# Optimization experiments

Hardware: AMD Instinct MI355X
Metric: run time of the kernel (lower is better)

The kernel has to match this reference:

```python
import jax, jax.numpy as jnp
import numpy as np


def setup_inputs() -> dict:
    key = jax.random.key(0)
    k1, k2, k3 = jax.random.split(key, 3)
    B, S, D_IN, D_OUT = 2, 2048, 4096, 4096
    x = jax.random.normal(k1, (B, S, D_IN), dtype=jnp.float32)
    # int8 quantized weight (stored as int32 container, values in int8 range)
    weight = jax.random.randint(k2, (D_OUT, D_IN), 0, 127, dtype=jnp.int32)
    weight_scaler = jax.random.uniform(k3, (D_OUT,), dtype=jnp.float32)
    return {"x": x, "weight": weight, "weight_scaler": weight_scaler}


def reference(x, weight, weight_scaler):
    # Dequantize per-output-channel: w_fp = int8_weight * scaler[:, None]
    w = weight.astype(jnp.float32) * weight_scaler[:, None]  # [O, I]
    # F.linear: x @ w.T
    return jnp.einsum("bsi,oi->bso", x, w)
```

## Files before the change

### kernel.cpp

```cpp
#include <hip/hip_runtime.h>

typedef int i32x4 __attribute__((ext_vector_type(4)));

#define AS1 __attribute__((address_space(1)))
#define AS3 __attribute__((address_space(3)))

__global__ __launch_bounds__(256) void quant_kernel(
    const float4* __restrict__ x, const int4* __restrict__ w,
    signed char* __restrict__ xq, signed char* __restrict__ wq,
    float* __restrict__ sx, int M, int Kq) {
  const int tid = threadIdx.x;
  if ((int)blockIdx.x < M) {
    const int r = blockIdx.x;
    float4 v[4];
    #pragma unroll
    for (int j = 0; j < 4; ++j) v[j] = x[(size_t)r * 1024 + tid * 4 + j];
    float m = 0.f;
    #pragma unroll
    for (int j = 0; j < 4; ++j)
      m = fmaxf(m, fmaxf(fmaxf(fabsf(v[j].x), fabsf(v[j].y)),
                         fmaxf(fabsf(v[j].z), fabsf(v[j].w))));
    #pragma unroll
    for (int off = 1; off < 64; off <<= 1) m = fmaxf(m, __shfl_xor(m, off));
    __shared__ float wmax[4];
    if ((tid & 63) == 0) wmax[tid >> 6] = m;
    __syncthreads();
    m = fmaxf(fmaxf(wmax[0], wmax[1]), fmaxf(wmax[2], wmax[3]));
    const float inv = (m > 0.f) ? 127.0f / m : 0.f;
    if (tid == 0) sx[r] = m * (1.0f / 127.0f);
    signed char q[16];
    #pragma unroll
    for (int j = 0; j < 4; ++j) {
      q[j * 4 + 0] = (signed char)__float2int_rn(v[j].x * inv);
      q[j * 4 + 1] = (signed char)__float2int_rn(v[j].y * inv);
      q[j * 4 + 2] = (signed char)__float2int_rn(v[j].z * inv);
      q[j * 4 + 3] = (signed char)__float2int_rn(v[j].w * inv);
    }
    ((int4*)xq)[(size_t)r * 256 + tid] = *(const int4*)q;
  } else {
    const int b = blockIdx.x - M;
    int4 v[4];
    #pragma unroll
    for (int j = 0; j < 4; ++j) v[j] = w[(size_t)b * 1024 + tid * 4 + j];
    signed char q[16];
    #pragma unroll
    for (int j = 0; j < 4; ++j) {
      q[j * 4 + 0] = (signed char)v[j].x; q[j * 4 + 1] = (signed char)v[j].y;
      q[j * 4 + 2] = (signed char)v[j].z; q[j * 4 + 3] = (signed char)v[j].w;
    }
    ((int4*)wq)[(size_t)b * 256 + tid] = *(const int4*)q;
  }
}

__global__ __launch_bounds__(512, 2) void gemm_i8_kernel(
    const signed char* __restrict__ A,
    const signed char* __restrict__ B,
    const float* __restrict__ sx,
    const float* __restrict__ scaler,
    float* __restrict__ C,
    int M, int N, int K)
{
  __shared__ signed char sA[4][256 * 64];
  __shared__ signed char sB[4][256 * 64];

  const int tid  = threadIdx.x;
  const int wave = tid >> 6;
  const int lane = tid & 63;
  const int bm = blockIdx.y << 8;
  const int bn = blockIdx.x << 8;

  const int wm = (wave >> 2) << 7;
  const int wn = (wave & 3) << 6;
  const int l15  = lane & 15;
  const int quad = lane >> 4;

  const int srow = tid >> 2;
  const int kg = (tid & 3) ^ ((srow >> 1) & 3);
  const signed char* ga = A + (size_t)(bm + srow) * K + kg * 16;
  const signed char* gb = B + (size_t)(bn + srow) * K + kg * 16;
  const size_t rstep = (size_t)128 * K;
  const int ldst = tid * 16;

  const int pk   = (quad ^ ((l15 >> 1) & 3)) << 4;
  const int aoff = (wm + l15) * 64 + pk;
  const int boff = (wn + l15) * 64 + pk;

  i32x4 acc[8][4] = {};

#define STAGE_A(tt) do { const int sb_ = (tt) & 3;                           \
    __builtin_amdgcn_global_load_lds((AS1 void*)(ga + (size_t)(tt) * 64),    \
                                     (AS3 void*)(&sA[sb_][ldst]), 16, 0, 0); \
    __builtin_amdgcn_global_load_lds((AS1 void*)(ga + (size_t)(tt) * 64 + rstep), \
                                     (AS3 void*)(&sA[sb_][8192 + ldst]), 16, 0, 0); } while (0)
#define STAGE_B(tt) do { const int sb_ = (tt) & 3;                           \
    __builtin_amdgcn_global_load_lds((AS1 void*)(gb + (size_t)(tt) * 64),    \
                                     (AS3 void*)(&sB[sb_][ldst]), 16, 0, 0); \
    __builtin_amdgcn_global_load_lds((AS1 void*)(gb + (size_t)(tt) * 64 + rstep), \
                                     (AS3 void*)(&sB[sb_][8192 + ldst]), 16, 0, 0); } while (0)

  const int nt = K >> 6;

  STAGE_A(0); STAGE_B(0); STAGE_A(1); STAGE_B(1);
  asm volatile("s_waitcnt vmcnt(4)" ::: "memory");
  __builtin_amdgcn_s_barrier();
  __builtin_amdgcn_sched_barrier(0);

  for (int t = 0; t < nt; ++t) {
    const signed char* la = sA[t & 3];
    const signed char* lb = sB[t & 3];
    const bool st = (t < nt - 2);
    i32x4 av[4], bv[4];

    if (st) STAGE_A(t + 2);
    #pragma unroll
    for (int ni = 0; ni < 4; ++ni) bv[ni] = *(const i32x4*)&lb[boff + ni * 1024];
    #pragma unroll
    for (int mi = 0; mi < 4; ++mi) av[mi] = *(const i32x4*)&la[aoff + mi * 1024];
    __builtin_amdgcn_s_barrier();
    __builtin_amdgcn_s_setprio(1);
    #pragma unroll
    for (int mi = 0; mi < 4; ++mi)
      #pragma unroll
      for (int ni = 0; ni < 4; ++ni)
        acc[mi][ni] = __builtin_amdgcn_mfma_i32_16x16x64_i8(av[mi], bv[ni], acc[mi][ni], 0, 0, 0);
    __builtin_amdgcn_s_setprio(0);
    __builtin_amdgcn_s_barrier();

    if (st) STAGE_B(t + 2);
    #pragma unroll
    for (int mi = 0; mi < 4; ++mi) av[mi] = *(const i32x4*)&la[aoff + (mi + 4) * 1024];
    __builtin_amdgcn_s_barrier();
    __builtin_amdgcn_s_setprio(1);
    #pragma unroll
    for (int mi = 0; mi < 4; ++mi)
      #pragma unroll
      for (int ni = 0; ni < 4; ++ni)
        acc[mi + 4][ni] = __builtin_amdgcn_mfma_i32_16x16x64_i8(av[mi], bv[ni], acc[mi + 4][ni], 0, 0, 0);
    __builtin_amdgcn_s_setprio(0);

    if (st)                 asm volatile("s_waitcnt vmcnt(4)" ::: "memory");
    else if (t == nt - 2)   asm volatile("s_waitcnt vmcnt(0)" ::: "memory");
    __builtin_amdgcn_s_barrier();
    __builtin_amdgcn_sched_barrier(0);
  }
#undef STAGE_A
#undef STAGE_B

  #pragma unroll
  for (int mi = 0; mi < 8; ++mi) {
    const int gm0 = bm + wm + mi * 16 + quad * 4;
    float sr[4];
    #pragma unroll
    for (int r = 0; r < 4; ++r) sr[r] = sx[gm0 + r];
    #pragma unroll
    for (int ni = 0; ni < 4; ++ni) {
      const int gn = bn + wn + ni * 16 + l15;
      const float sc = scaler[gn];
      #pragma unroll
      for (int r = 0; r < 4; ++r)
        C[(size_t)(gm0 + r) * N + gn] = (float)acc[mi][ni][r] * sr[r] * sc;
    }
  }
}

extern "C" void kernel_launch(void* const* d_in, const int* in_sizes, int n_in,
                              void* d_out, int out_size, void* d_ws, size_t ws_size,
                              hipStream_t stream) {
  const float* x  = (const float*)d_in[0];
  const int*   w  = (const int*)d_in[1];
  const float* sc = (const float*)d_in[2];
  float* out = (float*)d_out;

  const int N = in_sizes[2];
  const int K = in_sizes[1] / N;
  const int M = in_sizes[0] / K;

  signed char* Aq = (signed char*)d_ws;
  signed char* Bq = Aq + (size_t)M * K;
  float* sx = (float*)(Bq + (size_t)N * K);

  const int wBlocks = (N * K) / (256 * 16);
  quant_kernel<<<M + wBlocks, 256, 0, stream>>>(
      (const float4*)x, (const int4*)w, Aq, Bq, sx, M, K / 16);

  dim3 grid(N / 256, M / 256);
  gemm_i8_kernel<<<grid, 512, 0, stream>>>(Aq, Bq, sx, sc, out, M, N, K);
}
```

Before: 252.1 us.

## Deepen LDS prefetch to three stages and use one barrier per K-step

The int8 GEMM main loop now prefetches three K-tiles ahead into the four LDS buffers instead of two. It issues the A and B tile loads together, then loads all eight A fragments and runs all 32 MFMAs in one block. The four per-iteration barriers and the setprio toggles are replaced by a single waitcnt plus barrier. The aim is to hide more global-load latency and cut synchronisation overhead. In exchange it holds more VGPRs for the fragments and loses the split load/compute interleave across waves.

After: 251.2 us. About the same (-0.3%).

```diff
diff --git a/kernel.cpp b/kernel.cpp
--- a/kernel.cpp
+++ b/kernel.cpp
@@ -87,64 +87,46 @@
 
   i32x4 acc[8][4] = {};
 
-#define STAGE_A(tt) do { const int sb_ = (tt) & 3;                           \
-    __builtin_amdgcn_global_load_lds((AS1 void*)(ga + (size_t)(tt) * 64),    \
-                                     (AS3 void*)(&sA[sb_][ldst]), 16, 0, 0); \
-    __builtin_amdgcn_global_load_lds((AS1 void*)(ga + (size_t)(tt) * 64 + rstep), \
-                                     (AS3 void*)(&sA[sb_][8192 + ldst]), 16, 0, 0); } while (0)
-#define STAGE_B(tt) do { const int sb_ = (tt) & 3;                           \
-    __builtin_amdgcn_global_load_lds((AS1 void*)(gb + (size_t)(tt) * 64),    \
-                                     (AS3 void*)(&sB[sb_][ldst]), 16, 0, 0); \
-    __builtin_amdgcn_global_load_lds((AS1 void*)(gb + (size_t)(tt) * 64 + rstep), \
-                                     (AS3 void*)(&sB[sb_][8192 + ldst]), 16, 0, 0); } while (0)
+#define STAGE(tt) do { const int sb_ = (tt) & 3; const size_t ko_ = (size_t)(tt) * 64; \
+    __builtin_amdgcn_global_load_lds((AS1 void*)(ga + ko_),         (AS3 void*)(&sA[sb_][ldst]),        16, 0, 0); \
+    __builtin_amdgcn_global_load_lds((AS1 void*)(ga + ko_ + rstep), (AS3 void*)(&sA[sb_][8192 + ldst]), 16, 0, 0); \
+    __builtin_amdgcn_global_load_lds((AS1 void*)(gb + ko_),         (AS3 void*)(&sB[sb_][ldst]),        16, 0, 0); \
+    __builtin_amdgcn_global_load_lds((AS1 void*)(gb + ko_ + rstep), (AS3 void*)(&sB[sb_][8192 + ldst]), 16, 0, 0); } while (0)
 
   const int nt = K >> 6;
 
-  STAGE_A(0); STAGE_B(0); STAGE_A(1); STAGE_B(1);
-  asm volatile("s_waitcnt vmcnt(4)" ::: "memory");
+  STAGE(0); STAGE(1); STAGE(2);
+  asm volatile("s_waitcnt vmcnt(8)" ::: "memory");
   __builtin_amdgcn_s_barrier();
   __builtin_amdgcn_sched_barrier(0);
 
   for (int t = 0; t < nt; ++t) {
     const signed char* la = sA[t & 3];
     const signed char* lb = sB[t & 3];
-    const bool st = (t < nt - 2);
-    i32x4 av[4], bv[4];
 
-    if (st) STAGE_A(t + 2);
+    if (t < nt - 3) STAGE(t + 3);
+
+    i32x4 av[8], bv[4];
     #pragma unroll
     for (int ni = 0; ni < 4; ++ni) bv[ni] = *(const i32x4*)&lb[boff + ni * 1024];
     #pragma unroll
-    for (int mi = 0; mi < 4; ++mi) av[mi] = *(const i32x4*)&la[aoff + mi * 1024];
-    __builtin_amdgcn_s_barrier();
-    __builtin_amdgcn_s_setprio(1);
+    for (int mi = 0; mi < 8; ++mi) av[mi] = *(const i32x4*)&la[aoff + mi * 1024];
+
     #pragma unroll
-    for (int mi = 0; mi < 4; ++mi)
+    for (int mi = 0; mi < 8; ++mi)
       #pragma unroll
       for (int ni = 0; ni < 4; ++ni)
         acc[mi][ni] = __builtin_amdgcn_mfma_i32_16x16x64_i8(av[mi], bv[ni], acc[mi][ni], 0, 0, 0);
-    __builtin_amdgcn_s_setprio(0);
-    __builtin_amdgcn_s_barrier();
 
-    if (st) STAGE_B(t + 2);
-    #pragma unroll
-    for (int mi = 0; mi < 4; ++mi) av[mi] = *(const i32x4*)&la[aoff + (mi + 4) * 1024];
-    __builtin_amdgcn_s_barrier();
-    __builtin_amdgcn_s_setprio(1);
-    #pragma unroll
-    for (int mi = 0; mi < 4; ++mi)
-      #pragma unroll
-      for (int ni = 0; ni < 4; ++ni)
-        acc[mi + 4][ni] = __builtin_amdgcn_mfma_i32_16x16x64_i8(av[mi], bv[ni], acc[mi + 4][ni], 0, 0, 0);
-    __builtin_amdgcn_s_setprio(0);
-
-    if (st)                 asm volatile("s_waitcnt vmcnt(4)" ::: "memory");
-    else if (t == nt - 2)   asm volatile("s_waitcnt vmcnt(0)" ::: "memory");
-    __builtin_amdgcn_s_barrier();
-    __builtin_amdgcn_sched_barrier(0);
+    if (t < nt - 3)        asm volatile("s_waitcnt vmcnt(8)" ::: "memory");
+    else if (t == nt - 3)  asm volatile("s_waitcnt vmcnt(4)" ::: "memory");
+    else if (t == nt - 2)  asm volatile("s_waitcnt vmcnt(0)" ::: "memory");
+    if (t < nt - 1) {
+      __builtin_amdgcn_s_barrier();
+      __builtin_amdgcn_sched_barrier(0);
+    }
   }
-#undef STAGE_A
-#undef STAGE_B
+#undef STAGE
 
   #pragma unroll
   for (int mi = 0; mi < 8; ++mi) {
```
